# Kernel tuning notes

Measured on AMD Instinct MI355X. Metric: run time of the kernel, lower is better.

## Reference

```python
import jax, jax.numpy as jnp
import numpy as np

N = 100000      # num nodes
E = 800000      # num edges (avg degree 8)
D_IN = 128
D_OUT = 128
ALPHA = 0.5


def setup_inputs() -> dict:
    key = jax.random.key(0)
    ks = jax.random.split(key, 8)
    x = jax.random.normal(ks[0], (N, D_IN), dtype=jnp.float32)
    edge_index = jax.random.randint(ks[1], (2, E), 0, N, dtype=jnp.int64)
    s = 1.0 / np.sqrt(D_IN)
    # lin_self (nn.Linear), and per-direction SAGEConv lin_l (root_weight=False, bias=True)
    W_self = jax.random.uniform(ks[2], (D_IN, D_OUT), jnp.float32, -s, s)
    b_self = jax.random.uniform(ks[3], (D_OUT,), jnp.float32, -s, s)
    W_s2d = jax.random.uniform(ks[4], (D_IN, D_OUT), jnp.float32, -s, s)
    b_s2d = jnp.zeros((D_OUT,), jnp.float32)
    W_d2s = jax.random.uniform(ks[5], (D_IN, D_OUT), jnp.float32, -s, s)
    b_d2s = jnp.zeros((D_OUT,), jnp.float32)
    return {"x": x, "W_self": W_self, "b_self": b_self,
            "W_s2d": W_s2d, "b_s2d": b_s2d,
            "W_d2s": W_d2s, "b_d2s": b_d2s,
            "edge_index": edge_index}


def _mean_aggr(x, gather_idx, scatter_idx, num_nodes):
    # mean of x[gather_idx] segmented by scatter_idx; isolated nodes -> 0 (PyG scatter-mean semantics)
    summed = jax.ops.segment_sum(x[gather_idx], scatter_idx, num_segments=num_nodes)
    cnt = jax.ops.segment_sum(jnp.ones(gather_idx.shape, x.dtype), scatter_idx, num_segments=num_nodes)
    return summed / jnp.maximum(cnt, 1.0)[:, None]


def reference(x, W_self, b_self, W_s2d, b_s2d, W_d2s, b_d2s, edge_index):
    src, dst = edge_index[0], edge_index[1]
    n = x.shape[0]
    # flow='source_to_target': aggregate src features at dst (in-neighbors)
    agg_in = _mean_aggr(x, src, dst, n)
    # flow='target_to_source': aggregate dst features at src (out-neighbors)
    agg_out = _mean_aggr(x, dst, src, n)
    out = (x @ W_self + b_self
           + (1.0 - ALPHA) * (agg_in @ W_s2d + b_s2d)
           + ALPHA * (agg_out @ W_d2s + b_d2s))
    return out
```

## Files before the change

kernel.cpp:

```cpp
#include <hip/hip_runtime.h>


#define D 128
#define KTOT 384
#define NP 16
#define NPSH 4
#define RNGP 12500
#define NCH 48
#define TN 512
#define BT 512

typedef unsigned short u16;
typedef unsigned char u8;
typedef short bf16x8 __attribute__((ext_vector_type(8)));
typedef float f32x4 __attribute__((ext_vector_type(4)));
typedef float f32x2 __attribute__((ext_vector_type(2)));
typedef int i32x4 __attribute__((ext_vector_type(4)));

__device__ __forceinline__ u16 f2bf(float f) {
    unsigned u = __float_as_uint(f);
    unsigned r = (u + 0x7FFF + ((u >> 16) & 1)) >> 16;
    return (u16)r;
}

__device__ __forceinline__ unsigned cvt_pk_bf16(float a, float b) {
    unsigned r;
    asm("v_cvt_pk_bf16_f32 %0, %1, %2" : "=v"(r) : "v"(a), "v"(b));
    return r;
}

__global__ __launch_bounds__(256) void prep_w_k(const float* __restrict__ W0,
                                                const float* __restrict__ W1,
                                                const float* __restrict__ W2,
                                                const float* __restrict__ b0,
                                                const float* __restrict__ b1,
                                                const float* __restrict__ b2,
                                                u16* __restrict__ Wt,
                                                float* __restrict__ biasc) {
    int idx = blockIdx.x * 256 + threadIdx.x;
    if (idx < 128 * KTOT) {
        int n = idx / KTOT;
        int kt = idx - n * KTOT;
        int seg = kt >> 7;
        int k = kt & 127;
        const float* W = (seg == 0) ? W0 : (seg == 1) ? W1 : W2;
        Wt[n * KTOT + kt] = f2bf(W[k * D + n]);
    }
    if (idx < D) {
        biasc[idx] = b0[idx] + 0.5f * (b1[idx] + b2[idx]);
    }
}

__global__ __launch_bounds__(256) void conv_x_k(const float* __restrict__ x,
                                                u16* __restrict__ Ab,
                                                unsigned* __restrict__ xq,
                                                int N) {
    int gid = blockIdx.x * 256 + threadIdx.x;
    int node = gid >> 5;
    int c = gid & 31;
    if (node >= N) return;
    float4 v = *(const float4*)&x[(size_t)node * D + c * 4];
    ushort4 o;
    o.x = f2bf(v.x); o.y = f2bf(v.y); o.z = f2bf(v.z); o.w = f2bf(v.w);
    *(ushort4*)&Ab[(size_t)node * KTOT + c * 4] = o;
    int q = __builtin_amdgcn_cvt_pk_fp8_f32(v.x, v.y, 0, false);
    q = __builtin_amdgcn_cvt_pk_fp8_f32(v.z, v.w, q, true);
    xq[(size_t)node * 32 + c] = (unsigned)q;
}

__global__ __launch_bounds__(BT) void count_part_k(const int* __restrict__ ei,
                                                   int E, int N, int n2, int S2,
                                                   u8* __restrict__ deg2) {
    __shared__ unsigned cnt[RNGP / 4];
    const int p = blockIdx.x & (NP - 1);
    const int c = blockIdx.x >> NPSH;
    const int lo = p * RNGP;
    const int hi = min(n2, lo + RNGP);
    for (int i = threadIdx.x; i < RNGP / 4; i += BT) cnt[i] = 0;
    __syncthreads();

    const int pc = (((E + NCH - 1) / NCH) + 3) & ~3;
    const int beg = c * pc;
    const int end = min(E, beg + pc);
    for (int e = beg + ((int)threadIdx.x << 2); e < end; e += BT * 4) {
        if (e + 3 < end) {
            i32x4 s4 = __builtin_nontemporal_load((const i32x4*)&ei[e]);
            i32x4 d4 = __builtin_nontemporal_load((const i32x4*)&ei[E + e]);
#pragma unroll
            for (int j = 0; j < 4; ++j) {
                int d = d4[j];
                if (d >= lo && d < hi) {
                    int i = d - lo;
                    atomicAdd(&cnt[i >> 2], 1u << (8 * (i & 3)));
                }
                int os = N + s4[j];
                if (os >= lo && os < hi) {
                    int i = os - lo;
                    atomicAdd(&cnt[i >> 2], 1u << (8 * (i & 3)));
                }
            }
        } else {
            for (int j = 0; j < end - e; ++j) {
                int s = ei[e + j], d = ei[E + e + j];
                if (d >= lo && d < hi) {
                    int i = d - lo;
                    atomicAdd(&cnt[i >> 2], 1u << (8 * (i & 3)));
                }
                int os = N + s;
                if (os >= lo && os < hi) {
                    int i = os - lo;
                    atomicAdd(&cnt[i >> 2], 1u << (8 * (i & 3)));
                }
            }
        }
    }
    __syncthreads();
    unsigned* dst = (unsigned*)(deg2 + (size_t)c * S2 + lo);
    const int spanw = (hi - lo) >> 2;
    for (int i = threadIdx.x; i < spanw; i += BT) dst[i] = cnt[i];
}

__global__ __launch_bounds__(256) void rowscan_k(u8* __restrict__ deg2,
                                                 int* __restrict__ deg,
                                                 int n2, int S2) {
    __shared__ u8 t[NCH][TN];
    const int base = blockIdx.x * TN;
#pragma unroll
    for (int c = 0; c < NCH; ++c) {
        unsigned* src = (unsigned*)&deg2[(size_t)c * S2 + base];
        unsigned* dl = (unsigned*)&t[c][0];
        for (int i = threadIdx.x; i < TN / 4; i += 256) dl[i] = src[i];
    }
    __syncthreads();
    for (int j = threadIdx.x; j < TN; j += 256) {
        int run = 0;
#pragma unroll
        for (int c = 0; c < NCH; ++c) {
            int v = t[c][j];
            t[c][j] = (u8)run;
            run += v;
        }
        if (base + j < n2) deg[base + j] = run;
    }
    __syncthreads();
#pragma unroll
    for (int c = 0; c < NCH; ++c) {
        unsigned* dstg = (unsigned*)&deg2[(size_t)c * S2 + base];
        unsigned* sl = (unsigned*)&t[c][0];
        for (int i = threadIdx.x; i < TN / 4; i += 256) dstg[i] = sl[i];
    }
}

__device__ __forceinline__ int block_incl_scan(int v, int* wsum) {
    int lane = threadIdx.x & 63;
    int wv = threadIdx.x >> 6;
#pragma unroll
    for (int off = 1; off < 64; off <<= 1) {
        int t = __shfl_up(v, off, 64);
        if (lane >= off) v += t;
    }
    if (lane == 63) wsum[wv] = v;
    __syncthreads();
    int add = 0;
    for (int w = 0; w < wv; ++w) add += wsum[w];
    return v + add;
}

__global__ __launch_bounds__(256) void scan1_k(const int* __restrict__ in, int n,
                                               int* __restrict__ bsum) {
    __shared__ int wsum[4];
    int i = blockIdx.x * 256 + threadIdx.x;
    int v = (i < n) ? in[i] : 0;
    int s = block_incl_scan(v, wsum);
    if (threadIdx.x == 255) bsum[blockIdx.x] = s;
}

__global__ __launch_bounds__(1024) void scan2_k(int* __restrict__ bsum, int nb) {
    __shared__ int wsum[16];
    int i = threadIdx.x;
    int v = (i < nb) ? bsum[i] : 0;
    int s = block_incl_scan(v, wsum);
    if (i < nb) bsum[i] = s - v;
}

__global__ __launch_bounds__(256) void scan3_k(const int* __restrict__ in, int n,
                                               const int* __restrict__ bsum,
                                               int* __restrict__ ptr) {
    __shared__ int wsum[4];
    int i = blockIdx.x * 256 + threadIdx.x;
    int v = (i < n) ? in[i] : 0;
    int s = block_incl_scan(v, wsum);
    int off = bsum[blockIdx.x];
    if (i < n) ptr[i] = off + s - v;
    if (i == n - 1) ptr[n] = off + s;
}

__global__ __launch_bounds__(BT) void fill2_part_k(const int* __restrict__ ei,
                                                   int E, int N, int n2, int S2,
                                                   const int* __restrict__ ptr,
                                                   const u8* __restrict__ deg2,
                                                   int* __restrict__ adj) {
    __shared__ unsigned cnt[RNGP / 4];
    const int p = blockIdx.x & (NP - 1);
    const int c = blockIdx.x >> NPSH;
    const int lo = p * RNGP;
    const int hi = min(n2, lo + RNGP);
    const unsigned* d2w = (const unsigned*)(deg2 + (size_t)c * S2 + lo);
    for (int i = threadIdx.x; i < RNGP / 4; i += BT) cnt[i] = d2w[i];
    __syncthreads();

    const int pc = (((E + NCH - 1) / NCH) + 3) & ~3;
    const int beg = c * pc;
    const int end = min(E, beg + pc);
    for (int e = beg + ((int)threadIdx.x << 2); e < end; e += BT * 4) {
        if (e + 3 < end) {
            i32x4 s4 = __builtin_nontemporal_load((const i32x4*)&ei[e]);
            i32x4 d4 = __builtin_nontemporal_load((const i32x4*)&ei[E + e]);
#pragma unroll
            for (int j = 0; j < 4; ++j) {
                int s = s4[j], d = d4[j];
                if (d >= lo && d < hi) {
                    int i = d - lo;
                    unsigned old = atomicAdd(&cnt[i >> 2], 1u << (8 * (i & 3)));
                    int off = (int)((old >> (8 * (i & 3))) & 0xFFu);
                    adj[ptr[d] + off] = s;
                }
                int os = N + s;
                if (os >= lo && os < hi) {
                    int i = os - lo;
                    unsigned old = atomicAdd(&cnt[i >> 2], 1u << (8 * (i & 3)));
                    int off = (int)((old >> (8 * (i & 3))) & 0xFFu);
                    adj[ptr[os] + off] = d;
                }
            }
        } else {
            for (int j = 0; j < end - e; ++j) {
                int s = ei[e + j], d = ei[E + e + j];
                if (d >= lo && d < hi) {
                    int i = d - lo;
                    unsigned old = atomicAdd(&cnt[i >> 2], 1u << (8 * (i & 3)));
                    int off = (int)((old >> (8 * (i & 3))) & 0xFFu);
                    adj[ptr[d] + off] = s;
                }
                int os = N + s;
                if (os >= lo && os < hi) {
                    int i = os - lo;
                    unsigned old = atomicAdd(&cnt[i >> 2], 1u << (8 * (i & 3)));
                    int off = (int)((old >> (8 * (i & 3))) & 0xFFu);
                    adj[ptr[os] + off] = d;
                }
            }
        }
    }
}

__global__ __launch_bounds__(256) void agg_k(const unsigned* __restrict__ xq,
                                             u16* __restrict__ Ab,
                                             const int* __restrict__ ptr,
                                             const int* __restrict__ adj,
                                             int N) {
    int gid = blockIdx.x * 256 + threadIdx.x;
    int node = gid >> 3;
    int l8 = gid & 7;
    if (node >= N) return;
    const int dir = blockIdx.y;
    const int ci = dir * N + node;

    int beg = ptr[ci], end = ptr[ci + 1];
    f32x2 acc[8];
#pragma unroll
    for (int j = 0; j < 8; ++j) acc[j] = (f32x2){0.f, 0.f};

    for (int j0 = beg; j0 < end; j0 += 8) {
        int a = (j0 + l8 < end) ? adj[j0 + l8] : 0;
        int m = min(8, end - j0);
        for (int t = 0; t < m; ++t) {
            int nbr = __shfl(a, t, 8);
            uint4 q = *(const uint4*)((const char*)xq + ((size_t)nbr * 128 + l8 * 16));
            acc[0] += __builtin_amdgcn_cvt_pk_f32_fp8((int)q.x, false);
            acc[1] += __builtin_amdgcn_cvt_pk_f32_fp8((int)q.x, true);
            acc[2] += __builtin_amdgcn_cvt_pk_f32_fp8((int)q.y, false);
            acc[3] += __builtin_amdgcn_cvt_pk_f32_fp8((int)q.y, true);
            acc[4] += __builtin_amdgcn_cvt_pk_f32_fp8((int)q.z, false);
            acc[5] += __builtin_amdgcn_cvt_pk_f32_fp8((int)q.z, true);
            acc[6] += __builtin_amdgcn_cvt_pk_f32_fp8((int)q.w, false);
            acc[7] += __builtin_amdgcn_cvt_pk_f32_fp8((int)q.w, true);
        }
    }

    float s = 0.5f / fmaxf((float)(end - beg), 1.0f);
    unsigned w[8];
#pragma unroll
    for (int j = 0; j < 8; ++j)
        w[j] = cvt_pk_bf16(acc[j].x * s, acc[j].y * s);
    u16* dst = &Ab[(size_t)node * KTOT + 128 + dir * 128 + l8 * 16];
    *(uint4*)dst = make_uint4(w[0], w[1], w[2], w[3]);
    *(uint4*)(dst + 8) = make_uint4(w[4], w[5], w[6], w[7]);
}

#define BK 64
__global__ __launch_bounds__(256) void gemm_k(const u16* __restrict__ Ab,
                                              const u16* __restrict__ Wt,
                                              const float* __restrict__ biasc,
                                              float* __restrict__ out, int N) {
    __shared__ u16 As[64 * 72];
    __shared__ u16 Bs[128 * 72];

    const int tid = threadIdx.x;
    const int row0 = blockIdx.x * 64;
    const int w = tid >> 6;
    const int lane = tid & 63;
    const int m = lane & 15;
    const int quad = lane >> 4;

    f32x4 acc[8];
#pragma unroll
    for (int t = 0; t < 8; ++t) acc[t] = (f32x4){0.f, 0.f, 0.f, 0.f};

    for (int kb = 0; kb < KTOT / BK; ++kb) {
        const int k0 = kb * BK;
        __syncthreads();
#pragma unroll
        for (int i = 0; i < 2; ++i) {
            int f = tid + i * 256;
            int r = f >> 3;
            int q8 = f & 7;
            int grow = row0 + r;
            uint4 v = make_uint4(0u, 0u, 0u, 0u);
            if (grow < N)
                v = *(const uint4*)&Ab[(size_t)grow * KTOT + k0 + q8 * 8];
            *(uint4*)&As[r * 72 + q8 * 8] = v;
        }
#pragma unroll
        for (int i = 0; i < 4; ++i) {
            int f = tid + i * 256;
            int n = f >> 3;
            int q8 = f & 7;
            uint4 v = *(const uint4*)&Wt[(size_t)n * KTOT + k0 + q8 * 8];
            *(uint4*)&Bs[n * 72 + q8 * 8] = v;
        }
        __syncthreads();

        bf16x8 a[2];
#pragma unroll
        for (int s = 0; s < 2; ++s)
            a[s] = *(const bf16x8*)&As[(w * 16 + m) * 72 + s * 32 + quad * 8];
#pragma unroll
        for (int t = 0; t < 8; ++t) {
#pragma unroll
            for (int s = 0; s < 2; ++s) {
                bf16x8 b = *(const bf16x8*)&Bs[(t * 16 + m) * 72 + s * 32 + quad * 8];
                acc[t] = __builtin_amdgcn_mfma_f32_16x16x32_bf16(a[s], b, acc[t], 0, 0, 0);
            }
        }
    }

    const int rowbase = row0 + w * 16 + quad * 4;
#pragma unroll
    for (int t = 0; t < 8; ++t) {
        int col = t * 16 + m;
        float b = biasc[col];
#pragma unroll
        for (int r = 0; r < 4; ++r) {
            int row = rowbase + r;
            if (row < N) out[(size_t)row * D + col] = acc[t][r] + b;
        }
    }
}


extern "C" void kernel_launch(void* const* d_in, const int* in_sizes, int n_in,
                              void* d_out, int out_size, void* d_ws, size_t ws_size,
                              hipStream_t stream) {
    const float* x      = (const float*)d_in[0];
    const float* W_self = (const float*)d_in[1];
    const float* b_self = (const float*)d_in[2];
    const float* W_s2d  = (const float*)d_in[3];
    const float* b_s2d  = (const float*)d_in[4];
    const float* W_d2s  = (const float*)d_in[5];
    const float* b_d2s  = (const float*)d_in[6];
    const int*   ei     = (const int*)d_in[7];

    const int N = in_sizes[0] / D;
    const int E = in_sizes[7] / 2;
    float* out = (float*)d_out;
    char* ws = (char*)d_ws;

    const int n2 = 2 * N;
    const int S2 = ((n2 + TN - 1) / TN) * TN;

    size_t o = 0;
    u16* Ab = (u16*)(ws + o);        o += (size_t)N * KTOT * sizeof(u16);
    unsigned* xq = (unsigned*)(ws + o); o += (size_t)N * 32 * sizeof(unsigned);
    u16* Wt = (u16*)(ws + o);        o += (size_t)D * KTOT * sizeof(u16);
    float* biasc = (float*)(ws + o); o += D * sizeof(float);
    int* deg = (int*)(ws + o);       o += (size_t)n2 * sizeof(int);
    int* ptr = (int*)(ws + o);       o += ((size_t)n2 + 1) * sizeof(int);
    u8* deg2 = (u8*)(ws + o);        o += (size_t)NCH * S2 * sizeof(u8);
    int* adj = (int*)(ws + o);       o += (size_t)2 * E * sizeof(int);
    int* bs  = (int*)(ws + o);       o += 1024 * sizeof(int);

    const int nb2 = (n2 + 255) / 256;
    const int node32_blocks = (int)(((size_t)N * 32 + 255) / 256);
    const int node8_blocks = (int)(((size_t)N * 8 + 255) / 256);
    const int gemm_blocks = (N + 63) / 64;
    const int cs_grid = NCH * NP;
    const int rs_grid = S2 / TN;

    prep_w_k<<<(128 * KTOT + 255) / 256, 256, 0, stream>>>(W_self, W_s2d, W_d2s,
                                                           b_self, b_s2d, b_d2s,
                                                           Wt, biasc);
    conv_x_k<<<node32_blocks, 256, 0, stream>>>(x, Ab, xq, N);

    count_part_k<<<cs_grid, BT, 0, stream>>>(ei, E, N, n2, S2, deg2);
    rowscan_k<<<rs_grid, 256, 0, stream>>>(deg2, deg, n2, S2);
    scan1_k<<<nb2, 256, 0, stream>>>(deg, n2, bs);
    scan2_k<<<1, 1024, 0, stream>>>(bs, nb2);
    scan3_k<<<nb2, 256, 0, stream>>>(deg, n2, bs, ptr);
    fill2_part_k<<<cs_grid, BT, 0, stream>>>(ei, E, N, n2, S2, ptr, deg2, adj);

    dim3 agrid(node8_blocks, 2);
    agg_k<<<agrid, 256, 0, stream>>>(xq, Ab, ptr, adj, N);

    gemm_k<<<gemm_blocks, 256, 0, stream>>>(Ab, Wt, biasc, out, N);
}
```

Before: 262.5 us.

## Retile GEMM to 128x128 blocks with direct global-to-LDS loads

The fused GEMM now gives each block 128 rows instead of 64. The four waves are arranged 2x2, and each wave computes a 64x64 sub-tile from four A and four B fragments, so each LDS fragment load feeds more MFMAs. Tiles are staged with global_load_lds 16-byte transfers straight into unpadded LDS, removing the register round trip. The row bounds check on A loads is dropped, so the last block reads past N within the workspace, and the unpadded stride may add LDS bank conflicts.

```diff
diff --git a/kernel.cpp b/kernel.cpp
--- a/kernel.cpp
+++ b/kernel.cpp
@@ -27,6 +27,12 @@
     unsigned r;
     asm("v_cvt_pk_bf16_f32 %0, %1, %2" : "=v"(r) : "v"(a), "v"(b));
     return r;
+}
+
+__device__ __forceinline__ void gload_lds16(const void* g, void* l) {
+    __builtin_amdgcn_global_load_lds(
+        (const __attribute__((address_space(1))) unsigned*)g,
+        (__attribute__((address_space(3))) unsigned*)l, 16, 0, 0);
 }
 
 __global__ __launch_bounds__(256) void prep_w_k(const float* __restrict__ W0,
@@ -303,67 +309,77 @@
                                               const u16* __restrict__ Wt,
                                               const float* __restrict__ biasc,
                                               float* __restrict__ out, int N) {
-    __shared__ u16 As[64 * 72];
-    __shared__ u16 Bs[128 * 72];
+    __shared__ u16 As[128 * BK];
+    __shared__ u16 Bs[128 * BK];
 
     const int tid = threadIdx.x;
-    const int row0 = blockIdx.x * 64;
+    const int row0 = blockIdx.x * 128;
     const int w = tid >> 6;
     const int lane = tid & 63;
     const int m = lane & 15;
     const int quad = lane >> 4;
-
-    f32x4 acc[8];
-#pragma unroll
-    for (int t = 0; t < 8; ++t) acc[t] = (f32x4){0.f, 0.f, 0.f, 0.f};
+    const int wr = w >> 1;
+    const int wc = w & 1;
+
+    f32x4 acc[4][4];
+#pragma unroll
+    for (int i = 0; i < 4; ++i)
+#pragma unroll
+        for (int j = 0; j < 4; ++j) acc[i][j] = (f32x4){0.f, 0.f, 0.f, 0.f};
 
     for (int kb = 0; kb < KTOT / BK; ++kb) {
         const int k0 = kb * BK;
         __syncthreads();
 #pragma unroll
-        for (int i = 0; i < 2; ++i) {
-            int f = tid + i * 256;
-            int r = f >> 3;
-            int q8 = f & 7;
-            int grow = row0 + r;
-            uint4 v = make_uint4(0u, 0u, 0u, 0u);
-            if (grow < N)
-                v = *(const uint4*)&Ab[(size_t)grow * KTOT + k0 + q8 * 8];
-            *(uint4*)&As[r * 72 + q8 * 8] = v;
-        }
-#pragma unroll
         for (int i = 0; i < 4; ++i) {
-            int f = tid + i * 256;
-            int n = f >> 3;
-            int q8 = f & 7;
-            uint4 v = *(const uint4*)&Wt[(size_t)n * KTOT + k0 + q8 * 8];
-            *(uint4*)&Bs[n * 72 + q8 * 8] = v;
+            int ci = i * 256 + tid;
+            int r = ci >> 3;
+            int q8 = ci & 7;
+            gload_lds16(&Ab[(size_t)(row0 + r) * KTOT + k0 + q8 * 8],
+                        &As[(i * 256 + w * 64) * 8]);
+        }
+#pragma unroll
+        for (int i = 0; i < 4; ++i) {
+            int ci = i * 256 + tid;
+            int n = ci >> 3;
+            int q8 = ci & 7;
+            gload_lds16(&Wt[(size_t)n * KTOT + k0 + q8 * 8],
+                        &Bs[(i * 256 + w * 64) * 8]);
         }
         __syncthreads();
 
-        bf16x8 a[2];
-#pragma unroll
-        for (int s = 0; s < 2; ++s)
-            a[s] = *(const bf16x8*)&As[(w * 16 + m) * 72 + s * 32 + quad * 8];
-#pragma unroll
-        for (int t = 0; t < 8; ++t) {
-#pragma unroll
-            for (int s = 0; s < 2; ++s) {
-                bf16x8 b = *(const bf16x8*)&Bs[(t * 16 + m) * 72 + s * 32 + quad * 8];
-                acc[t] = __builtin_amdgcn_mfma_f32_16x16x32_bf16(a[s], b, acc[t], 0, 0, 0);
-            }
-        }
-    }
-
-    const int rowbase = row0 + w * 16 + quad * 4;
-#pragma unroll
-    for (int t = 0; t < 8; ++t) {
-        int col = t * 16 + m;
-        float b = biasc[col];
-#pragma unroll
-        for (int r = 0; r < 4; ++r) {
-            int row = rowbase + r;
-            if (row < N) out[(size_t)row * D + col] = acc[t][r] + b;
+        bf16x8 a[4][2], b[4][2];
+#pragma unroll
+        for (int i = 0; i < 4; ++i)
+#pragma unroll
+            for (int s = 0; s < 2; ++s)
+                a[i][s] = *(const bf16x8*)&As[(wr * 64 + i * 16 + m) * BK + s * 32 + quad * 8];
+#pragma unroll
+        for (int j = 0; j < 4; ++j)
+#pragma unroll
+            for (int s = 0; s < 2; ++s)
+                b[j][s] = *(const bf16x8*)&Bs[(wc * 64 + j * 16 + m) * BK + s * 32 + quad * 8];
+#pragma unroll
+        for (int i = 0; i < 4; ++i)
+#pragma unroll
+            for (int j = 0; j < 4; ++j) {
+                acc[i][j] = __builtin_amdgcn_mfma_f32_16x16x32_bf16(a[i][0], b[j][0], acc[i][j], 0, 0, 0);
+                acc[i][j] = __builtin_amdgcn_mfma_f32_16x16x32_bf16(a[i][1], b[j][1], acc[i][j], 0, 0, 0);
+            }
+    }
+
+#pragma unroll
+    for (int j = 0; j < 4; ++j) {
+        int col = wc * 64 + j * 16 + m;
+        float bv = biasc[col];
+#pragma unroll
+        for (int i = 0; i < 4; ++i) {
+            int rbase = row0 + wr * 64 + i * 16 + quad * 4;
+#pragma unroll
+            for (int r = 0; r < 4; ++r) {
+                int row = rbase + r;
+                if (row < N) out[(size_t)row * D + col] = acc[i][j][r] + bv;
+            }
         }
     }
 }
@@ -403,7 +419,7 @@
     const int nb2 = (n2 + 255) / 256;
     const int node32_blocks = (int)(((size_t)N * 32 + 255) / 256);
     const int node8_blocks = (int)(((size_t)N * 8 + 255) / 256);
-    const int gemm_blocks = (N + 63) / 64;
+    const int gemm_blocks = (N + 127) / 128;
     const int cs_grid = NCH * NP;
     const int rs_grid = S2 / TN;
 
```

After: 256.8 us. 2.2% less time.
